# Kernel optimization log

Measured on AMD Instinct MI355X. Metric: run time of the kernel, lower is better.

Reference implementation:

```python
import jax, jax.numpy as jnp
import numpy as np
import math

C = 768          # in_channels
KC = 768         # key_channels
VC = 768         # value_channels
H = 12           # head_count
B, N = 8, 2048


def setup_inputs() -> dict:
    key = jax.random.key(0)
    ks = jax.random.split(key, 9)
    s = 0.02
    return {
        "x": jax.random.normal(ks[0], (B, N, C), dtype=jnp.float32),
        # Linear weights stored as (in, out); y = x @ W + b
        "Wq": jax.random.normal(ks[1], (C, KC), dtype=jnp.float32) * s,
        "bq": jnp.zeros((KC,), dtype=jnp.float32),
        "Wk": jax.random.normal(ks[2], (C, KC), dtype=jnp.float32) * s,
        "bk": jnp.zeros((KC,), dtype=jnp.float32),
        "Wv": jax.random.normal(ks[3], (C, VC), dtype=jnp.float32) * s,
        "bv": jnp.zeros((VC,), dtype=jnp.float32),
        "Wr": jax.random.normal(ks[4], (VC, C), dtype=jnp.float32) * s,
        "br": jnp.zeros((C,), dtype=jnp.float32),
    }


def reference(x, Wq, bq, Wk, bk, Wv, bv, Wr, br):
    b, n, c = x.shape
    dk = KC // H  # head key channels
    dv = VC // H  # head value channels
    q = (x @ Wq + bq).reshape(b, n, H, dk)
    k = (x @ Wk + bk).reshape(b, n, H, dk)
    v = (x @ Wv + bv).reshape(b, n, H, dv)
    # NOTE: original scales by sqrt(N) (sequence length), not sqrt(d_head)
    scores = jnp.einsum("bqhd,bkhd->bhqk", q, k) / math.sqrt(n)
    attn = jax.nn.softmax(scores, axis=-1)
    out = jnp.einsum("bhqk,bkhd->bqhd", attn, v).reshape(b, n, VC)
    # reprojection + relu; dropout is identity in eval mode
    return jax.nn.relu(out @ Wr + br)
```

## Files before the change

kernel.cpp:

```cpp
#include <hip/hip_runtime.h>
#include <math.h>

typedef unsigned short u16;
typedef short short8 __attribute__((ext_vector_type(8)));
typedef float f32x4 __attribute__((ext_vector_type(4)));

#define BATCH 8
#define SEQ   2048
#define CH    768
#define NH    12
#define DH    64
#define BH    (BATCH*NH)
#define MTOT  (BATCH*SEQ)

#if __has_builtin(__builtin_amdgcn_exp2f)
#define EXP2F(x) __builtin_amdgcn_exp2f(x)
#else
#define EXP2F(x) exp2f(x)
#endif

#define GL2L(g, l) __builtin_amdgcn_global_load_lds( \
    (const __attribute__((address_space(1))) void*)(g), \
    (__attribute__((address_space(3))) void*)(l), 16, 0, 0)

#define BARRIER_FULL() asm volatile("s_waitcnt vmcnt(0) lgkmcnt(0)\n\ts_barrier" ::: "memory")

__device__ __forceinline__ float bf2f(u16 u) {
  union { unsigned int i; float f; } v; v.i = ((unsigned int)u) << 16; return v.f;
}
__device__ __forceinline__ u16 f2bf(float f) {
  union { float f; unsigned int i; } v; v.f = f;
  return (u16)((v.i + 0x7fffu + ((v.i >> 16) & 1u)) >> 16);
}

__global__ void sniff_k(const u16* __restrict__ x, int* __restrict__ flag) {
  __shared__ int cnt;
  if (threadIdx.x == 0) cnt = 0;
  __syncthreads();
  int big = 0;
  for (int i = 0; i < 8; ++i) {
    u16 u = x[threadIdx.x + i * 256];
    int e = (u >> 7) & 0xFF;
    if (e >= 0x89) big++;
  }
  atomicAdd(&cnt, big);
  __syncthreads();
  if (threadIdx.x == 0) *flag = (cnt > 4) ? 1 : 0;
}

__global__ __launch_bounds__(256) void cvt_x_k(const void* __restrict__ xin,
                                               u16* __restrict__ xb,
                                               const int* __restrict__ flag) {
  int i4 = (blockIdx.x * 256 + threadIdx.x) * 4;
  if (*flag) {
    float4 f = *(const float4*)((const float*)xin + i4);
    ushort4 o;
    o.x = f2bf(f.x); o.y = f2bf(f.y); o.z = f2bf(f.z); o.w = f2bf(f.w);
    *(ushort4*)(xb + i4) = o;
  } else {
    *(ushort4*)(xb + i4) = *(const ushort4*)((const u16*)xin + i4);
  }
}

__global__ void cvt_bias_k(const void* b0, const void* b1, const void* b2, const void* b3,
                           u16* __restrict__ biasb, const int* __restrict__ flag) {
  int isf = *flag;
  for (int t = threadIdx.x; t < 4 * CH; t += 256) {
    int wz = t / CH, c = t - wz * CH;
    const void* src = (wz == 0) ? b0 : (wz == 1) ? b1 : (wz == 2) ? b2 : b3;
    biasb[t] = isf ? f2bf(((const float*)src)[c]) : ((const u16*)src)[c];
  }
}

__global__ __launch_bounds__(256) void transpose_w4_k(u16* __restrict__ wt,
    const void* w0, const void* w1, const void* w2, const void* w3,
    const int* __restrict__ flag) {
  __shared__ __align__(16) u16 t[64][65];
  const int z = blockIdx.z;
  const void* in = (z == 0) ? w0 : (z == 1) ? w1 : (z == 2) ? w2 : w3;
  u16* out = wt + (size_t)z * CH * CH;
  const int tid = threadIdx.x;
  const int r0 = blockIdx.y * 64, c0 = blockIdx.x * 64;
  const int isf = *flag;
#pragma unroll
  for (int i = 0; i < 16; ++i) {
    int idx = i * 256 + tid;
    int row = idx >> 6, col = idx & 63;
    size_t g = (size_t)(r0 + row) * CH + c0 + col;
    t[row][col] = isf ? f2bf(((const float*)in)[g]) : ((const u16*)in)[g];
  }
  __syncthreads();
#pragma unroll
  for (int i = 0; i < 16; ++i) {
    int idx = i * 256 + tid;
    int orow = idx >> 6, ocol = idx & 63;
    out[(size_t)(c0 + orow) * CH + r0 + ocol] = t[ocol][orow];
  }
}

template <int EPI>
__global__ __launch_bounds__(256) void gemm_bt_k(
    const u16* __restrict__ A, const u16* __restrict__ BtBase,
    const u16* __restrict__ biasb, u16* __restrict__ outBase,
    u16* __restrict__ voutBase, void* __restrict__ finalOut,
    const int* __restrict__ flag, float qscale) {
  const int K = CH;
  const int tid = threadIdx.x;
  const int wv = tid >> 6, lane = tid & 63, quad = lane >> 4, l16 = lane & 15;
  const int wm = (wv >> 1) * 64, wn = (wv & 1) * 64;

  const int id = blockIdx.x;
  const int xcd = id & 7, u = id >> 3;
  int n0, m0, z;
  if (EPI == 0) {
    int n0z = u % 18, yl = u / 18;
    n0 = (n0z % 6) * 128; z = n0z / 6;
    m0 = (xcd + 8 * yl) * 128;
  } else {
    int n0z = u % 6, yl = u / 6;
    n0 = n0z * 128; z = 3;
    m0 = (xcd + 8 * yl) * 128;
  }
  const u16* Bt = BtBase + (size_t)z * CH * CH;
  const u16* bias = biasb + (size_t)z * CH;

  __shared__ __align__(16) u16 As[128 * 64];
  __shared__ __align__(16) u16 Bs[128 * 64];

  const f32x4 fz4 = {0.f, 0.f, 0.f, 0.f};
  f32x4 acc[4][4];
#pragma unroll
  for (int mt = 0; mt < 4; ++mt)
#pragma unroll
    for (int nt = 0; nt < 4; ++nt) acc[mt][nt] = fz4;

  for (int kt = 0; kt < K; kt += 64) {
#pragma unroll
    for (int i = 0; i < 4; ++i) {
      int c = tid + i * 256;
      int r = c >> 3;
      int pg = (c & 7) ^ (r & 7);
      GL2L(A + (size_t)(m0 + r) * K + kt + pg * 8, As + c * 8);
    }
#pragma unroll
    for (int i = 0; i < 4; ++i) {
      int c = tid + i * 256;
      int r = c >> 3;
      int pg = (c & 7) ^ (r & 7);
      GL2L(Bt + (size_t)(n0 + r) * K + kt + pg * 8, Bs + c * 8);
    }
    __syncthreads();

    short8 af[4][2], bf[4][2];
#pragma unroll
    for (int mt = 0; mt < 4; ++mt) {
      int r = wm + mt * 16 + l16;
#pragma unroll
      for (int ks = 0; ks < 2; ++ks) {
        int p = (ks * 4 + quad) ^ (r & 7);
        af[mt][ks] = *(const short8*)(As + r * 64 + p * 8);
      }
    }
#pragma unroll
    for (int nt = 0; nt < 4; ++nt) {
      int r = wn + nt * 16 + l16;
#pragma unroll
      for (int ks = 0; ks < 2; ++ks) {
        int p = (ks * 4 + quad) ^ (r & 7);
        bf[nt][ks] = *(const short8*)(Bs + r * 64 + p * 8);
      }
    }
#pragma unroll
    for (int ks = 0; ks < 2; ++ks)
#pragma unroll
      for (int mt = 0; mt < 4; ++mt)
#pragma unroll
        for (int nt = 0; nt < 4; ++nt)
          acc[mt][nt] = __builtin_amdgcn_mfma_f32_16x16x32_bf16(af[mt][ks], bf[nt][ks],
                                                                acc[mt][nt], 0, 0, 0);
    __syncthreads();
  }

  const int of32 = (EPI == 1) ? *flag : 0;
#pragma unroll
  for (int mt = 0; mt < 4; ++mt) {
#pragma unroll
    for (int nt = 0; nt < 4; ++nt) {
      int col = n0 + wn + nt * 16 + l16;
      float bv = bf2f(bias[col]);
      int rowb = m0 + wm + mt * 16 + quad * 4;
      if (EPI == 1) {
#pragma unroll
        for (int r = 0; r < 4; ++r) {
          float vv = fmaxf(acc[mt][nt][r] + bv, 0.0f);
          size_t off = (size_t)(rowb + r) * CH + col;
          if (of32) ((float*)finalOut)[off] = vv;
          else      ((u16*)finalOut)[off] = f2bf(vv);
        }
      } else if (z == 2) {
        int b = rowb >> 11, n = rowb & (SEQ - 1);
        int h = col >> 6, d = col & 63;
        ushort4 pk;
        pk.x = f2bf(acc[mt][nt][0] + bv);
        pk.y = f2bf(acc[mt][nt][1] + bv);
        pk.z = f2bf(acc[mt][nt][2] + bv);
        pk.w = f2bf(acc[mt][nt][3] + bv);
        *(ushort4*)(voutBase + ((size_t)((b * NH + h) * DH + d)) * SEQ + n) = pk;
      } else {
        float sc = (z == 0) ? qscale : 1.0f;
#pragma unroll
        for (int r = 0; r < 4; ++r) {
          float vv = (acc[mt][nt][r] + bv) * sc;
          int row = rowb + r;
          int b = row >> 11, n = row & (SEQ - 1);
          int h = col >> 6, d = col & 63;
          outBase[(size_t)z * BH * SEQ * DH + ((size_t)(b * NH + h) * SEQ + n) * DH + d] = f2bf(vv);
        }
      }
    }
  }
}

__global__ __launch_bounds__(256, 3) void flash_attn_k(
    const u16* __restrict__ Qg, const u16* __restrict__ Kg,
    const u16* __restrict__ Vtg, u16* __restrict__ Og) {
  const int tid = threadIdx.x;
  const int wv = tid >> 6, lane = tid & 63, quad = lane >> 4, l16 = lane & 15;
  const int id = blockIdx.x;
  const int bh = (id & 7) + 8 * (id >> 7);
  const int q0 = ((id >> 3) & 15) * 128;
  const int b = bh / NH, h = bh - b * NH;

  __shared__ __align__(16) u16 smem[24576];
  u16* Ps = smem + 16384;

  const f32x4 fz4 = {0.f, 0.f, 0.f, 0.f};

  const u16* Qp = Qg + (size_t)bh * SEQ * DH + (size_t)q0 * DH;
  const u16* Kp = Kg + (size_t)bh * SEQ * DH;
  const u16* Vp = Vtg + (size_t)bh * DH * SEQ;

#pragma unroll
  for (int i = 0; i < 4; ++i) {
    int c = tid + i * 256; int r = c >> 3; int pg = (c & 7) ^ (r & 7);
    GL2L(Qp + (size_t)r * DH + pg * 8, Ps + c * 8);
  }
#pragma unroll
  for (int i = 0; i < 2; ++i) {
    int c = tid + i * 256; int r = c >> 3; int pg = (c & 7) ^ (r & 7);
    GL2L(Kp + (size_t)r * DH + pg * 8, smem + c * 8);
    GL2L(Vp + (size_t)r * SEQ + pg * 8, smem + 4096 + c * 8);
  }
  __syncthreads();

  short8 qf[2][2];
#pragma unroll
  for (int mt = 0; mt < 2; ++mt) {
    int r = wv * 32 + mt * 16 + l16;
#pragma unroll
    for (int ks = 0; ks < 2; ++ks) {
      int p = (ks * 4 + quad) ^ (r & 7);
      qf[mt][ks] = *(const short8*)(Ps + r * 64 + p * 8);
    }
  }

  float lsum[2] = {0.f, 0.f};
  f32x4 oacc[2][4];
#pragma unroll
  for (int mt = 0; mt < 2; ++mt)
#pragma unroll
    for (int dt = 0; dt < 4; ++dt) oacc[mt][dt] = fz4;

  int cur = 0;
  for (int k0 = 0; k0 < SEQ; k0 += 64) {
    BARRIER_FULL();
    u16* Ks = smem + cur * 8192;
    u16* Vs = Ks + 4096;
    if (k0 + 64 < SEQ) {
      int k1 = k0 + 64;
      u16* Kn = smem + (cur ^ 1) * 8192;
#pragma unroll
      for (int i = 0; i < 2; ++i) {
        int c = tid + i * 256; int r = c >> 3; int pg = (c & 7) ^ (r & 7);
        GL2L(Kp + (size_t)(k1 + r) * DH + pg * 8, Kn + c * 8);
        GL2L(Vp + (size_t)r * SEQ + k1 + pg * 8, Kn + 4096 + c * 8);
      }
    }

    f32x4 s[2][4];
#pragma unroll
    for (int mt = 0; mt < 2; ++mt)
#pragma unroll
      for (int nt = 0; nt < 4; ++nt) s[mt][nt] = fz4;
#pragma unroll
    for (int nt = 0; nt < 4; ++nt) {
      int r = nt * 16 + l16;
#pragma unroll
      for (int ks = 0; ks < 2; ++ks) {
        int p = (ks * 4 + quad) ^ (r & 7);
        short8 kf = *(const short8*)(Ks + r * 64 + p * 8);
        s[0][nt] = __builtin_amdgcn_mfma_f32_16x16x32_bf16(kf, qf[0][ks], s[0][nt], 0, 0, 0);
        s[1][nt] = __builtin_amdgcn_mfma_f32_16x16x32_bf16(kf, qf[1][ks], s[1][nt], 0, 0, 0);
      }
    }

#pragma unroll
    for (int mt = 0; mt < 2; ++mt) {
      int row = wv * 32 + mt * 16 + l16;
      u16* prow = Ps + row * 64 + (quad & 1) * 4;
      int sw = row & 7;
#pragma unroll
      for (int nt = 0; nt < 4; ++nt) {
        float p0 = EXP2F(s[mt][nt][0]);
        float p1 = EXP2F(s[mt][nt][1]);
        float p2 = EXP2F(s[mt][nt][2]);
        float p3 = EXP2F(s[mt][nt][3]);
        lsum[mt] += (p0 + p1) + (p2 + p3);
        uint2 w;
        w.x = __builtin_amdgcn_perm(__float_as_uint(p1), __float_as_uint(p0), 0x07060302u);
        w.y = __builtin_amdgcn_perm(__float_as_uint(p3), __float_as_uint(p2), 0x07060302u);
        int c16 = (nt * 2 + (quad >> 1)) ^ sw;
        *(uint2*)(prow + c16 * 8) = w;
      }
    }
    asm volatile("" ::: "memory");

#pragma unroll
    for (int ks = 0; ks < 2; ++ks) {
      short8 pf[2];
#pragma unroll
      for (int mt = 0; mt < 2; ++mt) {
        int r = wv * 32 + mt * 16 + l16;
        int p = (ks * 4 + quad) ^ (r & 7);
        pf[mt] = *(const short8*)(Ps + r * 64 + p * 8);
      }
#pragma unroll
      for (int dt = 0; dt < 4; ++dt) {
        int rv = dt * 16 + l16;
        int p = (ks * 4 + quad) ^ (rv & 7);
        short8 vf = *(const short8*)(Vs + rv * 64 + p * 8);
        oacc[0][dt] = __builtin_amdgcn_mfma_f32_16x16x32_bf16(pf[0], vf, oacc[0][dt], 0, 0, 0);
        oacc[1][dt] = __builtin_amdgcn_mfma_f32_16x16x32_bf16(pf[1], vf, oacc[1][dt], 0, 0, 0);
      }
    }
    cur ^= 1;
  }

#pragma unroll
  for (int mt = 0; mt < 2; ++mt) {
    float v = lsum[mt];
    v += __shfl_xor(v, 16, 64);
    v += __shfl_xor(v, 32, 64);
    lsum[mt] = 1.0f / v;
  }

#pragma unroll
  for (int mt = 0; mt < 2; ++mt)
#pragma unroll
    for (int r = 0; r < 4; ++r) {
      float inv = __shfl(lsum[mt], quad * 4 + r, 16);
      int qi = q0 + wv * 32 + mt * 16 + quad * 4 + r;
      size_t base = ((size_t)(b * SEQ) + qi) * CH + h * DH;
#pragma unroll
      for (int dt = 0; dt < 4; ++dt) {
        int d = dt * 16 + l16;
        Og[base + d] = f2bf(oacc[mt][dt][r] * inv);
      }
    }
}

extern "C" void kernel_launch(void* const* d_in, const int* in_sizes, int n_in,
                              void* d_out, int out_size, void* d_ws, size_t ws_size,
                              hipStream_t stream) {
  const void* x  = d_in[0];
  const void* Wq = d_in[1];
  const void* bq = d_in[2];
  const void* Wk = d_in[3];
  const void* bk = d_in[4];
  const void* Wv = d_in[5];
  const void* bv = d_in[6];
  const void* Wr = d_in[7];
  const void* br = d_in[8];
  u16* ws = (u16*)d_ws;

  const size_t WSZ = (size_t)CH * CH;
  const size_t XSZ = (size_t)MTOT * CH;
  int* flag  = (int*)ws;
  u16* biasb = ws + 8;
  u16* wt    = ws + 4096;
  u16* xb    = wt + 4 * WSZ;
  u16* q     = xb + XSZ;
  u16* k     = q + XSZ;
  u16* vt    = k + XSZ;

  const float qscale = (float)(1.4426950408889634 / sqrt(2048.0));

  sniff_k<<<1, 256, 0, stream>>>((const u16*)x, flag);
  cvt_x_k<<<XSZ / 1024, 256, 0, stream>>>(x, xb, flag);
  cvt_bias_k<<<1, 256, 0, stream>>>(bq, bk, bv, br, biasb, flag);
  transpose_w4_k<<<dim3(12, 12, 4), 256, 0, stream>>>(wt, Wq, Wk, Wv, Wr, flag);
  gemm_bt_k<0><<<dim3(2304), 256, 0, stream>>>(xb, wt, biasb, q, vt, nullptr,
                                               flag, qscale);
  u16* ao = xb;
  flash_attn_k<<<dim3(1536), 256, 0, stream>>>(q, k, vt, ao);
  gemm_bt_k<1><<<dim3(768), 256, 0, stream>>>(ao, wt, biasb, nullptr, nullptr,
                                              d_out, flag, 1.0f);
}
```

Measured before the change: 371.6 us.

## Keep softmax probabilities in registers by permuting V layout to match MFMA operands

The attention kernel no longer writes the exponentiated scores to LDS and reads them back as MFMA A operands. It packs them directly into registers, relying on a permuted key ordering within each 32-column group of V^T, which the projection epilogue now writes. This removes the P staging buffer (shrinking LDS from 48KB to 32KB) and its LDS traffic. The smaller footprint allows raising launch bounds to 4 blocks per SM, at the risk of register pressure, and correctness depends on the permutation matching the MFMA lane mapping exactly.

```diff
diff --git a/kernel.cpp b/kernel.cpp
--- a/kernel.cpp
+++ b/kernel.cpp
@@ -200,12 +200,15 @@
       } else if (z == 2) {
         int b = rowb >> 11, n = rowb & (SEQ - 1);
         int h = col >> 6, d = col & 63;
+        int k5 = n & 31;
+        int sig = (((k5 & 15) >> 2) << 3) | ((k5 & 16) >> 2);
+        int np = (n & ~31) | sig;
         ushort4 pk;
         pk.x = f2bf(acc[mt][nt][0] + bv);
         pk.y = f2bf(acc[mt][nt][1] + bv);
         pk.z = f2bf(acc[mt][nt][2] + bv);
         pk.w = f2bf(acc[mt][nt][3] + bv);
-        *(ushort4*)(voutBase + ((size_t)((b * NH + h) * DH + d)) * SEQ + n) = pk;
+        *(ushort4*)(voutBase + ((size_t)((b * NH + h) * DH + d)) * SEQ + np) = pk;
       } else {
         float sc = (z == 0) ? qscale : 1.0f;
 #pragma unroll
@@ -221,7 +224,7 @@
   }
 }
 
-__global__ __launch_bounds__(256, 3) void flash_attn_k(
+__global__ __launch_bounds__(256, 4) void flash_attn_k(
     const u16* __restrict__ Qg, const u16* __restrict__ Kg,
     const u16* __restrict__ Vtg, u16* __restrict__ Og) {
   const int tid = threadIdx.x;
@@ -231,8 +234,7 @@
   const int q0 = ((id >> 3) & 15) * 128;
   const int b = bh / NH, h = bh - b * NH;
 
-  __shared__ __align__(16) u16 smem[24576];
-  u16* Ps = smem + 16384;
+  __shared__ __align__(16) u16 smem[16384];
 
   const f32x4 fz4 = {0.f, 0.f, 0.f, 0.f};
 
@@ -243,7 +245,7 @@
 #pragma unroll
   for (int i = 0; i < 4; ++i) {
     int c = tid + i * 256; int r = c >> 3; int pg = (c & 7) ^ (r & 7);
-    GL2L(Qp + (size_t)r * DH + pg * 8, Ps + c * 8);
+    GL2L(Qp + (size_t)r * DH + pg * 8, smem + 8192 + c * 8);
   }
 #pragma unroll
   for (int i = 0; i < 2; ++i) {
@@ -260,7 +262,7 @@
 #pragma unroll
     for (int ks = 0; ks < 2; ++ks) {
       int p = (ks * 4 + quad) ^ (r & 7);
-      qf[mt][ks] = *(const short8*)(Ps + r * 64 + p * 8);
+      qf[mt][ks] = *(const short8*)(smem + 8192 + r * 64 + p * 8);
     }
   }
 
@@ -304,43 +306,38 @@
       }
     }
 
+    short8 pf[2][2];
 #pragma unroll
     for (int mt = 0; mt < 2; ++mt) {
-      int row = wv * 32 + mt * 16 + l16;
-      u16* prow = Ps + row * 64 + (quad & 1) * 4;
-      int sw = row & 7;
-#pragma unroll
-      for (int nt = 0; nt < 4; ++nt) {
-        float p0 = EXP2F(s[mt][nt][0]);
-        float p1 = EXP2F(s[mt][nt][1]);
-        float p2 = EXP2F(s[mt][nt][2]);
-        float p3 = EXP2F(s[mt][nt][3]);
-        lsum[mt] += (p0 + p1) + (p2 + p3);
-        uint2 w;
-        w.x = __builtin_amdgcn_perm(__float_as_uint(p1), __float_as_uint(p0), 0x07060302u);
-        w.y = __builtin_amdgcn_perm(__float_as_uint(p3), __float_as_uint(p2), 0x07060302u);
-        int c16 = (nt * 2 + (quad >> 1)) ^ sw;
-        *(uint2*)(prow + c16 * 8) = w;
-      }
-    }
-    asm volatile("" ::: "memory");
+#pragma unroll
+      for (int ks = 0; ks < 2; ++ks) {
+        float p0 = EXP2F(s[mt][2 * ks][0]);
+        float p1 = EXP2F(s[mt][2 * ks][1]);
+        float p2 = EXP2F(s[mt][2 * ks][2]);
+        float p3 = EXP2F(s[mt][2 * ks][3]);
+        float p4 = EXP2F(s[mt][2 * ks + 1][0]);
+        float p5 = EXP2F(s[mt][2 * ks + 1][1]);
+        float p6 = EXP2F(s[mt][2 * ks + 1][2]);
+        float p7 = EXP2F(s[mt][2 * ks + 1][3]);
+        lsum[mt] += ((p0 + p1) + (p2 + p3)) + ((p4 + p5) + (p6 + p7));
+        union { unsigned int u[4]; short8 s8; } cv;
+        cv.u[0] = __builtin_amdgcn_perm(__float_as_uint(p1), __float_as_uint(p0), 0x07060302u);
+        cv.u[1] = __builtin_amdgcn_perm(__float_as_uint(p3), __float_as_uint(p2), 0x07060302u);
+        cv.u[2] = __builtin_amdgcn_perm(__float_as_uint(p5), __float_as_uint(p4), 0x07060302u);
+        cv.u[3] = __builtin_amdgcn_perm(__float_as_uint(p7), __float_as_uint(p6), 0x07060302u);
+        pf[mt][ks] = cv.s8;
+      }
+    }
 
 #pragma unroll
     for (int ks = 0; ks < 2; ++ks) {
-      short8 pf[2];
-#pragma unroll
-      for (int mt = 0; mt < 2; ++mt) {
-        int r = wv * 32 + mt * 16 + l16;
-        int p = (ks * 4 + quad) ^ (r & 7);
-        pf[mt] = *(const short8*)(Ps + r * 64 + p * 8);
-      }
 #pragma unroll
       for (int dt = 0; dt < 4; ++dt) {
         int rv = dt * 16 + l16;
         int p = (ks * 4 + quad) ^ (rv & 7);
         short8 vf = *(const short8*)(Vs + rv * 64 + p * 8);
-        oacc[0][dt] = __builtin_amdgcn_mfma_f32_16x16x32_bf16(pf[0], vf, oacc[0][dt], 0, 0, 0);
-        oacc[1][dt] = __builtin_amdgcn_mfma_f32_16x16x32_bf16(pf[1], vf, oacc[1][dt], 0, 0, 0);
+        oacc[0][dt] = __builtin_amdgcn_mfma_f32_16x16x32_bf16(pf[0][ks], vf, oacc[0][dt], 0, 0, 0);
+        oacc[1][dt] = __builtin_amdgcn_mfma_f32_16x16x32_bf16(pf[1][ks], vf, oacc[1][dt], 0, 0, 0);
       }
     }
     cur ^= 1;
```

Result: faster. 358.9 us (-3.4%).
